# Kernel tuning notes

Hardware: AMD Instinct MI355X
Metric: run time of the kernel (lower is better)

## Reference

```python
import jax, jax.numpy as jnp
import numpy as np
import math

N, S, E, BS = 8, 8192, 256, 8


def setup_inputs() -> dict:
    key = jax.random.key(0)
    k1, k2, k3 = jax.random.split(key, 3)
    seq_vector = jax.random.normal(k1, (N, S, E), dtype=jnp.float32)
    # Conv1d weight [target_dim, source_dim] (kernel size 1 squeezed), default torch init scale
    bound = 1.0 / math.sqrt(E)
    W = jax.random.uniform(k2, (E, E), minval=-bound, maxval=bound, dtype=jnp.float32)
    sigma = math.sqrt(1.0 / (BS * E))
    bias = jax.random.uniform(k3, (BS,), minval=-sigma, maxval=sigma, dtype=jnp.float32)
    return {"seq_vector": seq_vector, "W": W, "bias": bias}


def reference(seq_vector, W, bias):
    n, s, e = seq_vector.shape
    bs = bias.shape[0]
    # 1x1 conv == per-token projection: [N,S,E] x [T,E] -> [N,S,T]
    features = jnp.einsum('nse,te->nst', seq_vector, W)
    # group sequence into blocks: [N, S//bs, bs, T]
    fb = features.reshape(n, s // bs, bs, -1)
    # blockwise causal (strictly lower-triangular) sum == exclusive cumsum over block dim
    excl = jnp.cumsum(fb, axis=2) - fb
    # position i gets bias[i]; position 0 additionally gets bias[0] a second time
    b_eff = bias.at[0].add(bias[0])  # [bs]
    out = excl + b_eff[None, None, :, None]
    return out.reshape(n, s, -1)
```

## Files before the change

kernel.cpp:

```cpp
#include <hip/hip_runtime.h>


typedef short short8 __attribute__((ext_vector_type(8)));
typedef short short4v __attribute__((ext_vector_type(4)));
typedef float floatx4 __attribute__((ext_vector_type(4)));
typedef unsigned short ushort4v __attribute__((ext_vector_type(4)));

__device__ __forceinline__ unsigned short f2bf(float f) {
    union { float f; unsigned int u; } v;
    v.f = f;
    unsigned int u = v.u + 0x7fffu + ((v.u >> 16) & 1u);
    return (unsigned short)(u >> 16);
}

__device__ __forceinline__ short4v pack4(float4 f) {
    short4v r;
    r[0] = (short)f2bf(f.x); r[1] = (short)f2bf(f.y);
    r[2] = (short)f2bf(f.z); r[3] = (short)f2bf(f.w);
    return r;
}

__global__ __launch_bounds__(256) void wconv_kernel(
    const float* __restrict__ W, unsigned short* __restrict__ Wb)
{
    const int i = (blockIdx.x * 256 + threadIdx.x) * 4;
    float4 f = *(const float4*)(W + i);
    const int n = i >> 8, k = i & 255;
    const int idx =
        (((n >> 4) * 8 + (k >> 5)) * 64 + (n & 15) * 4 + ((k >> 3) & 3)) * 8 +
        (k & 7);
    ushort4v v;
    v[0] = f2bf(f.x); v[1] = f2bf(f.y); v[2] = f2bf(f.z); v[3] = f2bf(f.w);
    *(ushort4v*)(Wb + idx) = v;
}

__global__ __launch_bounds__(512, 4) void bcl_gemm_kernel(
    const float* __restrict__ X, const unsigned short* __restrict__ Wb,
    const float* __restrict__ bias, float* __restrict__ out)
{
    __shared__ unsigned short aT[2][32 * 256];
    __shared__ float epi[32 * 256];

    const int tid  = threadIdx.x;
    const int lane = tid & 63;
    const int w    = tid >> 6;
    const int cl   = lane & 15;
    const int q    = lane >> 4;

    short8 Bf[2][8];
    #pragma unroll
    for (int nt = 0; nt < 2; ++nt)
        #pragma unroll
        for (int kc = 0; kc < 8; ++kc)
            Bf[nt][kc] = *(const short8*)
                (Wb + ((((w * 2 + nt) * 8 + kc) * 64) + cl * 4 + q) * 8);

    const int tile0 = blockIdx.x * 4;
    float4 sF[4];

#define LOADT(tt)                                                             \
    do {                                                                      \
        const float* _g = X + (size_t)(tt) * 8192 + tid * 4;                  \
        _Pragma("unroll")                                                     \
        for (int _j = 0; _j < 4; ++_j)                                        \
            sF[_j] = *(const float4*)(_g + _j * 2048);                        \
    } while (0)

#define WRITET(b)                                                             \
    do {                                                                      \
        _Pragma("unroll")                                                     \
        for (int _j = 0; _j < 4; ++_j) {                                      \
            const int _row = _j * 8 + w;                                      \
            const int _ph  = (lane >> 1) ^ w;                 \
            *(short4v*)&aT[b][_row * 256 + _ph * 8 + (lane & 1) * 4] =        \
                pack4(sF[_j]);                                                \
        }                                                                     \
    } while (0)

#define COMPUTE(b)                                                            \
    do {                                                                      \
        _Pragma("unroll")                                                     \
        for (int kc = 0; kc < 8; ++kc) {                                      \
            _Pragma("unroll")                                                 \
            for (int mt = 0; mt < 2; ++mt) {                                  \
                short8 _a = *(const short8*)                                  \
                    &aT[b][(mt * 16 + cl) * 256 +                             \
                           (((kc * 4 + q) ^ (cl & 7)) << 3)];                 \
                acc[mt][0] = __builtin_amdgcn_mfma_f32_16x16x32_bf16(         \
                    _a, Bf[0][kc], acc[mt][0], 0, 0, 0);                      \
                acc[mt][1] = __builtin_amdgcn_mfma_f32_16x16x32_bf16(         \
                    _a, Bf[1][kc], acc[mt][1], 0, 0, 0);                      \
            }                                                                 \
        }                                                                     \
    } while (0)

    float be[4];
    {
        const int off = (q & 1) * 4;
        be[0] = bias[off + 0];
        be[1] = bias[off + 1];
        be[2] = bias[off + 2];
        be[3] = bias[off + 3];
        if (off == 0) be[0] += bias[0];
    }

    floatx4 acc[2][2];

    LOADT(tile0);
    WRITET(0);
    __syncthreads();

    #pragma unroll
    for (int t = 0; t < 4; ++t) {
        const int tile = tile0 + t;
        if (t + 1 < 4) LOADT(tile + 1);

        #pragma unroll
        for (int mt = 0; mt < 2; ++mt)
            #pragma unroll
            for (int nt = 0; nt < 2; ++nt)
                acc[mt][nt] = (floatx4){0.f, 0.f, 0.f, 0.f};

        COMPUTE(t & 1);
        if (t + 1 < 4) WRITET((t + 1) & 1);

        #pragma unroll
        for (int mt = 0; mt < 2; ++mt)
            #pragma unroll
            for (int nt = 0; nt < 2; ++nt) {
                floatx4 v = acc[mt][nt];
                float p1 = v[0];
                float p2 = p1 + v[1];
                float p3 = p2 + v[2];
                float tot = p3 + v[3];
                float below = __shfl_up(tot, 16);
                float p0 = 0.f;
                if (q & 1) { p0 = below; p1 += below; p2 += below; p3 += below; }
                const int rbase = mt * 16 + q * 4;
                const int ph = (w * 8 + nt * 4 + (cl >> 2)) ^ (q << 2);
                float* dst = &epi[rbase * 256 + ph * 4 + (cl & 3)];
                dst[0]   = p0 + be[0];
                dst[256] = p1 + be[1];
                dst[512] = p2 + be[2];
                dst[768] = p3 + be[3];
            }
        __syncthreads();

        #pragma unroll
        for (int k = 0; k < 4; ++k) {
            const int row = w * 4 + k;
            floatx4 vv = *(const floatx4*)
                &epi[row * 256 + ((lane ^ ((w & 3) << 2)) << 2)];
            *(floatx4*)&out[(size_t)(tile * 32 + row) * 256 + lane * 4] = vv;
        }
        if (t + 1 < 4) __syncthreads();
    }
#undef LOADT
#undef WRITET
#undef COMPUTE
}

extern "C" void kernel_launch(void* const* d_in, const int* in_sizes, int n_in,
                              void* d_out, int out_size, void* d_ws, size_t ws_size,
                              hipStream_t stream)
{
    const float* X = (const float*)d_in[0];
    const float* W = (const float*)d_in[1];
    const float* B = (const float*)d_in[2];
    float* out = (float*)d_out;
    unsigned short* Wb = (unsigned short*)d_ws;

    wconv_kernel<<<dim3(64), dim3(256), 0, stream>>>(W, Wb);
    bcl_gemm_kernel<<<dim3(512), dim3(512), 0, stream>>>(X, Wb, B, out);
}
```

Before: 123.9 us.

## Deepen X prefetch to two tiles with triple-buffered LDS and lighter barriers

The four-tile loop is fully unrolled into an explicit schedule. Global loads for tile t+2 are issued while tile t computes, using two register staging sets and three LDS input buffers. The __syncthreads calls are replaced by an LDS-only waitcnt plus s_barrier, so outstanding global loads no longer stall at each barrier. This keeps more memory traffic in flight for a bandwidth-bound kernel. In exchange it uses more LDS and registers per block, and the launch-bound occupancy hint drops from 4 to 3.

```diff
diff --git a/kernel.cpp b/kernel.cpp
--- a/kernel.cpp
+++ b/kernel.cpp
@@ -5,6 +5,12 @@
 typedef short short4v __attribute__((ext_vector_type(4)));
 typedef float floatx4 __attribute__((ext_vector_type(4)));
 typedef unsigned short ushort4v __attribute__((ext_vector_type(4)));
+
+#define LGKM0_BAR()                                                           \
+    do {                                                                      \
+        __builtin_amdgcn_s_waitcnt(0xC07F);                                   \
+        __builtin_amdgcn_s_barrier();                                         \
+    } while (0)
 
 __device__ __forceinline__ unsigned short f2bf(float f) {
     union { float f; unsigned int u; } v;
@@ -34,11 +40,11 @@
     *(ushort4v*)(Wb + idx) = v;
 }
 
-__global__ __launch_bounds__(512, 4) void bcl_gemm_kernel(
+__global__ __launch_bounds__(512, 3) void bcl_gemm_kernel(
     const float* __restrict__ X, const unsigned short* __restrict__ Wb,
     const float* __restrict__ bias, float* __restrict__ out)
 {
-    __shared__ unsigned short aT[2][32 * 256];
+    __shared__ unsigned short aT[3][32 * 256];
     __shared__ float epi[32 * 256];
 
     const int tid  = threadIdx.x;
@@ -56,41 +62,82 @@
                 (Wb + ((((w * 2 + nt) * 8 + kc) * 64) + cl * 4 + q) * 8);
 
     const int tile0 = blockIdx.x * 4;
-    float4 sF[4];
+    float4 sF[2][4];
 
 #define LOADT(tt)                                                             \
     do {                                                                      \
-        const float* _g = X + (size_t)(tt) * 8192 + tid * 4;                  \
+        const float* _g = X + (size_t)(tile0 + (tt)) * 8192 + tid * 4;        \
         _Pragma("unroll")                                                     \
         for (int _j = 0; _j < 4; ++_j)                                        \
-            sF[_j] = *(const float4*)(_g + _j * 2048);                        \
-    } while (0)
-
-#define WRITET(b)                                                             \
+            sF[(tt) & 1][_j] = *(const float4*)(_g + _j * 2048);              \
+    } while (0)
+
+#define WRITET(tt)                                                            \
     do {                                                                      \
         _Pragma("unroll")                                                     \
         for (int _j = 0; _j < 4; ++_j) {                                      \
             const int _row = _j * 8 + w;                                      \
-            const int _ph  = (lane >> 1) ^ w;                 \
-            *(short4v*)&aT[b][_row * 256 + _ph * 8 + (lane & 1) * 4] =        \
-                pack4(sF[_j]);                                                \
+            const int _ph  = (lane >> 1) ^ w;                                 \
+            *(short4v*)&aT[(tt) % 3][_row * 256 + _ph * 8 + (lane & 1) * 4]   \
+                = pack4(sF[(tt) & 1][_j]);                                    \
         }                                                                     \
     } while (0)
 
-#define COMPUTE(b)                                                            \
-    do {                                                                      \
-        _Pragma("unroll")                                                     \
-        for (int kc = 0; kc < 8; ++kc) {                                      \
+#define COMPUTE(tt)                                                           \
+    do {                                                                      \
+        _Pragma("unroll")                                                     \
+        for (int mt = 0; mt < 2; ++mt)                                        \
+            _Pragma("unroll")                                                 \
+            for (int nt = 0; nt < 2; ++nt)                                    \
+                acc[mt][nt] = (floatx4){0.f, 0.f, 0.f, 0.f};                  \
+        _Pragma("unroll")                                                     \
+        for (int kc = 0; kc < 8; ++kc)                                        \
             _Pragma("unroll")                                                 \
             for (int mt = 0; mt < 2; ++mt) {                                  \
                 short8 _a = *(const short8*)                                  \
-                    &aT[b][(mt * 16 + cl) * 256 +                             \
-                           (((kc * 4 + q) ^ (cl & 7)) << 3)];                 \
+                    &aT[(tt) % 3][(mt * 16 + cl) * 256 +                      \
+                                  (((kc * 4 + q) ^ (cl & 7)) << 3)];          \
                 acc[mt][0] = __builtin_amdgcn_mfma_f32_16x16x32_bf16(         \
                     _a, Bf[0][kc], acc[mt][0], 0, 0, 0);                      \
                 acc[mt][1] = __builtin_amdgcn_mfma_f32_16x16x32_bf16(         \
                     _a, Bf[1][kc], acc[mt][1], 0, 0, 0);                      \
             }                                                                 \
+    } while (0)
+
+#define EPI(tt)                                                               \
+    do {                                                                      \
+        _Pragma("unroll")                                                     \
+        for (int mt = 0; mt < 2; ++mt)                                        \
+            _Pragma("unroll")                                                 \
+            for (int nt = 0; nt < 2; ++nt) {                                  \
+                floatx4 v = acc[mt][nt];                                      \
+                float p1 = v[0];                                              \
+                float p2 = p1 + v[1];                                         \
+                float p3 = p2 + v[2];                                         \
+                float tot = p3 + v[3];                                        \
+                float below = __shfl_up(tot, 16);                             \
+                float p0 = 0.f;                                               \
+                if (q & 1) { p0 = below; p1 += below; p2 += below;            \
+                             p3 += below; }                                   \
+                const int rbase = mt * 16 + q * 4;                            \
+                const int ph = (w * 8 + nt * 4 + (cl >> 2)) ^ (q << 2);       \
+                float* dst = &epi[rbase * 256 + ph * 4 + (cl & 3)];           \
+                dst[0]   = p0 + be[0];                                        \
+                dst[256] = p1 + be[1];                                        \
+                dst[512] = p2 + be[2];                                        \
+                dst[768] = p3 + be[3];                                        \
+            }                                                                 \
+    } while (0)
+
+#define RBSTORE(tt)                                                           \
+    do {                                                                      \
+        _Pragma("unroll")                                                     \
+        for (int _k = 0; _k < 4; ++_k) {                                      \
+            const int _row = w * 4 + _k;                                      \
+            floatx4 vv = *(const floatx4*)                                    \
+                &epi[_row * 256 + ((lane ^ ((w & 3) << 2)) << 2)];            \
+            *(floatx4*)&out[(size_t)((tile0 + (tt)) * 32 + _row) * 256 +      \
+                            lane * 4] = vv;                                   \
         }                                                                     \
     } while (0)
 
@@ -106,58 +153,44 @@
 
     floatx4 acc[2][2];
 
-    LOADT(tile0);
+    LOADT(0);
+    LOADT(1);
     WRITET(0);
-    __syncthreads();
-
-    #pragma unroll
-    for (int t = 0; t < 4; ++t) {
-        const int tile = tile0 + t;
-        if (t + 1 < 4) LOADT(tile + 1);
-
-        #pragma unroll
-        for (int mt = 0; mt < 2; ++mt)
-            #pragma unroll
-            for (int nt = 0; nt < 2; ++nt)
-                acc[mt][nt] = (floatx4){0.f, 0.f, 0.f, 0.f};
-
-        COMPUTE(t & 1);
-        if (t + 1 < 4) WRITET((t + 1) & 1);
-
-        #pragma unroll
-        for (int mt = 0; mt < 2; ++mt)
-            #pragma unroll
-            for (int nt = 0; nt < 2; ++nt) {
-                floatx4 v = acc[mt][nt];
-                float p1 = v[0];
-                float p2 = p1 + v[1];
-                float p3 = p2 + v[2];
-                float tot = p3 + v[3];
-                float below = __shfl_up(tot, 16);
-                float p0 = 0.f;
-                if (q & 1) { p0 = below; p1 += below; p2 += below; p3 += below; }
-                const int rbase = mt * 16 + q * 4;
-                const int ph = (w * 8 + nt * 4 + (cl >> 2)) ^ (q << 2);
-                float* dst = &epi[rbase * 256 + ph * 4 + (cl & 3)];
-                dst[0]   = p0 + be[0];
-                dst[256] = p1 + be[1];
-                dst[512] = p2 + be[2];
-                dst[768] = p3 + be[3];
-            }
-        __syncthreads();
-
-        #pragma unroll
-        for (int k = 0; k < 4; ++k) {
-            const int row = w * 4 + k;
-            floatx4 vv = *(const floatx4*)
-                &epi[row * 256 + ((lane ^ ((w & 3) << 2)) << 2)];
-            *(floatx4*)&out[(size_t)(tile * 32 + row) * 256 + lane * 4] = vv;
-        }
-        if (t + 1 < 4) __syncthreads();
-    }
+    LGKM0_BAR();
+
+    LOADT(2);
+    COMPUTE(0);
+    WRITET(1);
+    LGKM0_BAR();
+    EPI(0);
+    LGKM0_BAR();
+    RBSTORE(0);
+
+    LOADT(3);
+    COMPUTE(1);
+    WRITET(2);
+    LGKM0_BAR();
+    EPI(1);
+    LGKM0_BAR();
+    RBSTORE(1);
+
+    COMPUTE(2);
+    WRITET(3);
+    LGKM0_BAR();
+    EPI(2);
+    LGKM0_BAR();
+    RBSTORE(2);
+
+    COMPUTE(3);
+    LGKM0_BAR();
+    EPI(3);
+    LGKM0_BAR();
+    RBSTORE(3);
 #undef LOADT
 #undef WRITET
 #undef COMPUTE
+#undef EPI
+#undef RBSTORE
 }
 
 extern "C" void kernel_launch(void* const* d_in, const int* in_sizes, int n_in,
```

After: 123.2 us. No clear change (-0.5%).
